# Kernel optimization log

Measured on AMD Instinct MI355X. Metric: run time of the kernel, lower is better.

## Reference

```python
import jax, jax.numpy as jnp
import numpy as np
from jax import lax


def setup_inputs() -> dict:
    key = jax.random.key(0)
    t_in = jax.random.normal(key, (16, 65536, 3), dtype=jnp.float32)
    return {"npoints": 2048, "t_in": t_in}


def reference(npoints, t_in):
    """Iterative farthest point sampling.

    t_in: (b, n, 3) float32 point coordinates.
    Returns (b, npoints) int32 indices of sampled points.
    Matches the PointNet++ CUDA kernel semantics: first sample is index 0,
    running min-distance buffer initialized to a large value, each step
    picks the argmax of the min-distance to the already-selected set.
    """
    b, n, p = t_in.shape
    assert p == 3
    BIG = jnp.float32(1e10)

    batch_ix = jnp.arange(b)

    def step(carry, _):
        dist, last_idx = carry                      # dist: (b,n), last_idx: (b,)
        last = t_in[batch_ix, last_idx]             # (b,3) last selected points
        d = jnp.sum((t_in - last[:, None, :]) ** 2, axis=-1)  # (b,n)
        dist = jnp.minimum(dist, d)
        nxt = jnp.argmax(dist, axis=-1).astype(jnp.int32)      # (b,)
        return (dist, nxt), nxt

    init_idx = jnp.zeros((b,), dtype=jnp.int32)
    dist0 = jnp.full((b, n), BIG, dtype=jnp.float32)
    (_, _), idxs = lax.scan(step, (dist0, init_idx), None, length=npoints - 1)
    # idxs: (npoints-1, b) -> (b, npoints-1)
    out = jnp.concatenate([init_idx[:, None], idxs.T], axis=1)  # (b, npoints)
    return out
```

## Files before the change

### kernel.cpp

```cpp
#include <hip/hip_runtime.h>
#include <stdint.h>


#define NBATCH   16
#define NPTS     65536
#define NPOINTS  2048
#define KBLK     16
#define THREADS  256
#define PPB      4096
#define PPT      16
#define SLOT_U64 8
#define REGION_U64 (KBLK * SLOT_U64)

#define TAGOK(w) (((unsigned)((w) >> 16) & 0xFFFFu) == tag)

typedef unsigned int uint4v __attribute__((ext_vector_type(4)));

__device__ __forceinline__ void load_slot16(const unsigned long long* p,
                                            unsigned long long& w0,
                                            unsigned long long& w1) {
    uint4v r;
    asm volatile("global_load_dwordx4 %0, %1, off sc0 sc1\n\t"
                 "s_waitcnt vmcnt(0)"
                 : "=v"(r) : "v"(p) : "memory");
    w0 = ((unsigned long long)r.y << 32) | r.x;
    w1 = ((unsigned long long)r.w << 32) | r.z;
}

__global__ __launch_bounds__(THREADS, 1)
void fps_kernel(const float* __restrict__ pts, int* __restrict__ out,
                unsigned long long* __restrict__ slots)
{
    const int bid  = blockIdx.x;
    const int g    = bid & 15;
    const int blk  = bid >> 4;
    const int tid  = threadIdx.x;
    const int lane = tid & 63;
    const int wave = tid >> 6;

    const float* __restrict__ P = pts + (size_t)g * (NPTS * 3);

    __shared__ unsigned long long s_mail[2][4];
    __shared__ unsigned long long s_cand[2][3][2];

    float  x[PPT], y[PPT], z[PPT];
    double dist[PPT];
    const int base = blk * PPB;
#pragma unroll
    for (int j = 0; j < PPT; ++j) {
        const int idx = base + j * THREADS + tid;
        x[j] = P[idx * 3 + 0];
        y[j] = P[idx * 3 + 1];
        z[j] = P[idx * 3 + 2];
        dist[j] = 1e10;
    }
    if (tid < 12) ((unsigned long long*)s_cand)[tid] = 0ull;
    if (tid < 8)  ((unsigned long long*)s_mail)[tid] = 0ull;
    __syncthreads();

    double qx = (double)P[0], qy = (double)P[1], qz = (double)P[2];
    if (blk == 0 && tid == 0) out[g * NPOINTS] = 0;

    for (int it = 0; it < NPOINTS - 1; ++it) {
        double bd = -1.0;
        int    bi = 0x7FFFFFFF;
        {
#pragma clang fp contract(off)
#pragma unroll
            for (int j = 0; j < PPT; ++j) {
                const double dx = (double)x[j] - qx;
                const double dy = (double)y[j] - qy;
                const double dz = (double)z[j] - qz;
                const double d  = (dx * dx + dy * dy) + dz * dz;
                const double nd = fmin(dist[j], d);
                dist[j] = nd;
                const bool t = nd > bd;
                bd = t ? nd : bd;
                bi = t ? (base + j * THREADS + tid) : bi;
            }
        }

#pragma unroll
        for (int m = 1; m < 64; m <<= 1) {
            const double od = __shfl_xor(bd, m, 64);
            const int    oi = __shfl_xor(bi, m, 64);
            const bool t = (od > bd) || (od == bd && oi < bi);
            bd = t ? od : bd; bi = t ? oi : bi;
        }

        const unsigned tag = (unsigned)(it + 1);
        const int par = it & 1;
        unsigned long long* rb =
            slots + (size_t)(par * NBATCH + g) * REGION_U64;

        float qxf, qyf, qzf;

        if (wave != 0) {
            if (lane == 0) {
                const unsigned long long B =
                    (unsigned long long)__double_as_longlong(bd);
                const unsigned long long TI =
                      ((unsigned long long)tag << 16)
                    | (unsigned long long)((unsigned)bi & 0xFFFFu);
                __hip_atomic_store(&s_cand[par][wave - 1][0],
                                   ((B >> 32) << 32) | TI,
                                   __ATOMIC_RELAXED,
                                   __HIP_MEMORY_SCOPE_WORKGROUP);
                __hip_atomic_store(&s_cand[par][wave - 1][1],
                                   ((B & 0xFFFFFFFFull) << 32) | TI,
                                   __ATOMIC_RELAXED,
                                   __HIP_MEMORY_SCOPE_WORKGROUP);
            }
            unsigned long long f1, f2, f3;
            int guard = 0;
            bool okm;
            do {
                f1 = __hip_atomic_load(&s_mail[par][0], __ATOMIC_RELAXED,
                                       __HIP_MEMORY_SCOPE_WORKGROUP);
                f2 = __hip_atomic_load(&s_mail[par][1], __ATOMIC_RELAXED,
                                       __HIP_MEMORY_SCOPE_WORKGROUP);
                f3 = __hip_atomic_load(&s_mail[par][2], __ATOMIC_RELAXED,
                                       __HIP_MEMORY_SCOPE_WORKGROUP);
                okm = ((unsigned)f1 == tag) & ((unsigned)f2 == tag)
                    & ((unsigned)f3 == tag);
            } while (!okm && ++guard < (1 << 20));
            qxf = __int_as_float((int)(f1 >> 32));
            qyf = __int_as_float((int)(f2 >> 32));
            qzf = __int_as_float((int)(f3 >> 32));
        } else {
            unsigned long long c[3][2];
            {
                int guard = 0;
                bool all;
                do {
                    all = true;
#pragma unroll
                    for (int w = 0; w < 3; ++w) {
                        c[w][0] = __hip_atomic_load(&s_cand[par][w][0],
                                      __ATOMIC_RELAXED,
                                      __HIP_MEMORY_SCOPE_WORKGROUP);
                        c[w][1] = __hip_atomic_load(&s_cand[par][w][1],
                                      __ATOMIC_RELAXED,
                                      __HIP_MEMORY_SCOPE_WORKGROUP);
                        all = all & TAGOK(c[w][0]) & TAGOK(c[w][1]);
                    }
                } while (!all && ++guard < (1 << 20));
            }
#pragma unroll
            for (int w = 0; w < 3; ++w) {
                const double od = __longlong_as_double((long long)(
                    ((c[w][0] >> 32) << 32) | (c[w][1] >> 32)));
                const int    oi = (int)(c[w][0] & 0xFFFFull);
                const bool t = (od > bd) || (od == bd && oi < bi);
                bd = t ? od : bd; bi = t ? oi : bi;
            }

            const unsigned long long B =
                (unsigned long long)__double_as_longlong(bd);
            const unsigned long long TI =
                  ((unsigned long long)tag << 16)
                | (unsigned long long)((unsigned)bi & 0xFFFFu);
            const unsigned long long own0 = ((B >> 32) << 32) | TI;
            const unsigned long long own1 = ((B & 0xFFFFFFFFull) << 32) | TI;

            if (lane < 2) {
                __hip_atomic_store(rb + blk * SLOT_U64 + lane,
                                   (lane == 0) ? own0 : own1,
                                   __ATOMIC_RELAXED,
                                   __HIP_MEMORY_SCOPE_AGENT);
            }

            unsigned long long* sp = rb + (lane & 15) * SLOT_U64;
            const bool own = ((lane & 15) == blk);
            unsigned long long l0 = own0, l1 = own1;
            bool ok = own;
            __builtin_amdgcn_s_sleep(12);
            int g1 = 0;
            while (!ok && g1 < 32) {
                load_slot16(sp, l0, l1);
                ok = TAGOK(l0) & TAGOK(l1);
                ++g1;
            }
            int g2 = 0;
            while (!ok) {
                l0 = __hip_atomic_load(sp + 0, __ATOMIC_RELAXED,
                                       __HIP_MEMORY_SCOPE_AGENT);
                l1 = __hip_atomic_load(sp + 1, __ATOMIC_RELAXED,
                                       __HIP_MEMORY_SCOPE_AGENT);
                ok = TAGOK(l0) & TAGOK(l1);
                if (++g2 > (1 << 20)) break;
            }

            double cd = __longlong_as_double(
                (long long)(((l0 >> 32) << 32) | (l1 >> 32)));
            int    ci = (int)(l0 & 0xFFFFull);

            const int    si = ci;
            const float* pc = P + (size_t)(unsigned)si * 3;
            const float px = pc[0];
            const float py = pc[1];
            const float pz = pc[2];

#pragma unroll
            for (int m = 1; m < 16; m <<= 1) {
                const double od = __shfl_xor(cd, m, 64);
                const int    oi = __shfl_xor(ci, m, 64);
                const bool t = (od > cd) || (od == cd && oi < ci);
                cd = t ? od : cd; ci = t ? oi : ci;
            }

            if (lane == 0 && blk == 0) out[g * NPOINTS + it + 1] = ci;

            const unsigned long long mb = __ballot(si == ci);
            const int wl = (__ffsll(mb) - 1) & 63;
            qxf = __int_as_float(
                __builtin_amdgcn_readlane(__float_as_int(px), wl));
            qyf = __int_as_float(
                __builtin_amdgcn_readlane(__float_as_int(py), wl));
            qzf = __int_as_float(
                __builtin_amdgcn_readlane(__float_as_int(pz), wl));

            if (lane < 3) {
                const unsigned coord =
                    (lane == 0) ? (unsigned)__float_as_int(qxf)
                  : (lane == 1) ? (unsigned)__float_as_int(qyf)
                                : (unsigned)__float_as_int(qzf);
                __hip_atomic_store(&s_mail[par][lane],
                                   ((unsigned long long)coord << 32)
                                 | (unsigned long long)tag,
                                   __ATOMIC_RELAXED,
                                   __HIP_MEMORY_SCOPE_WORKGROUP);
            }
        }

        qx = (double)qxf; qy = (double)qyf; qz = (double)qzf;
    }
}

extern "C" void kernel_launch(void* const* d_in, const int* in_sizes, int n_in,
                              void* d_out, int out_size, void* d_ws, size_t ws_size,
                              hipStream_t stream) {
    (void)in_sizes; (void)n_in; (void)out_size; (void)ws_size;
    const float* t_in = (const float*)d_in[1];
    int* out = (int*)d_out;
    unsigned long long* slots = (unsigned long long*)d_ws;

    dim3 grid(NBATCH * KBLK);
    dim3 block(THREADS);
    void* args[] = { (void*)&t_in, (void*)&out, (void*)&slots };
    hipLaunchCooperativeKernel((const void*)fps_kernel, grid, block, args, 0, stream);
}
```

Baseline: 4.771 ms.

## Publish per-wave candidates directly to global slots, skipping intra-block LDS merge

Each wave now writes its own argmax candidate to a global slot (16 blocks x 4 waves), and wave 0 of every block reads all 64 slots, one per lane, then reduces across the full wavefront. This drops the LDS handoff from waves 1-3 to wave 0, along with its spin wait, from the per-iteration critical path. Point coordinates are also pre-converted to double and kept in registers. The cost is four times as many global slots to poll, a full 64-lane reduction, and roughly double the register use for coordinates.

After: 4.431 ms. 1.08x faster.

```diff
diff --git a/kernel.cpp b/kernel.cpp
--- a/kernel.cpp
+++ b/kernel.cpp
@@ -9,8 +9,9 @@
 #define THREADS  256
 #define PPB      4096
 #define PPT      16
-#define SLOT_U64 8
-#define REGION_U64 (KBLK * SLOT_U64)
+#define QPB      4
+#define SLOT_U64 2
+#define REGION_U64 (KBLK * QPB * SLOT_U64)
 
 #define TAGOK(w) (((unsigned)((w) >> 16) & 0xFFFFu) == tag)
 
@@ -41,21 +42,18 @@
     const float* __restrict__ P = pts + (size_t)g * (NPTS * 3);
 
     __shared__ unsigned long long s_mail[2][4];
-    __shared__ unsigned long long s_cand[2][3][2];
-
-    float  x[PPT], y[PPT], z[PPT];
-    double dist[PPT];
+
+    double xd[PPT], yd[PPT], zd[PPT], dist[PPT];
     const int base = blk * PPB;
 #pragma unroll
     for (int j = 0; j < PPT; ++j) {
         const int idx = base + j * THREADS + tid;
-        x[j] = P[idx * 3 + 0];
-        y[j] = P[idx * 3 + 1];
-        z[j] = P[idx * 3 + 2];
+        xd[j] = (double)P[idx * 3 + 0];
+        yd[j] = (double)P[idx * 3 + 1];
+        zd[j] = (double)P[idx * 3 + 2];
         dist[j] = 1e10;
     }
-    if (tid < 12) ((unsigned long long*)s_cand)[tid] = 0ull;
-    if (tid < 8)  ((unsigned long long*)s_mail)[tid] = 0ull;
+    if (tid < 8) ((unsigned long long*)s_mail)[tid] = 0ull;
     __syncthreads();
 
     double qx = (double)P[0], qy = (double)P[1], qz = (double)P[2];
@@ -68,9 +66,9 @@
 #pragma clang fp contract(off)
 #pragma unroll
             for (int j = 0; j < PPT; ++j) {
-                const double dx = (double)x[j] - qx;
-                const double dy = (double)y[j] - qy;
-                const double dz = (double)z[j] - qz;
+                const double dx = xd[j] - qx;
+                const double dy = yd[j] - qy;
+                const double dz = zd[j] - qz;
                 const double d  = (dx * dx + dy * dy) + dz * dz;
                 const double nd = fmin(dist[j], d);
                 dist[j] = nd;
@@ -93,24 +91,24 @@
         unsigned long long* rb =
             slots + (size_t)(par * NBATCH + g) * REGION_U64;
 
+        const unsigned long long B =
+            (unsigned long long)__double_as_longlong(bd);
+        const unsigned long long TI =
+              ((unsigned long long)tag << 16)
+            | (unsigned long long)((unsigned)bi & 0xFFFFu);
+        const unsigned long long own0 = ((B >> 32) << 32) | TI;
+        const unsigned long long own1 = ((B & 0xFFFFFFFFull) << 32) | TI;
+
+        if (lane < 2) {
+            __hip_atomic_store(rb + (blk * QPB + wave) * SLOT_U64 + lane,
+                               (lane == 0) ? own0 : own1,
+                               __ATOMIC_RELAXED,
+                               __HIP_MEMORY_SCOPE_AGENT);
+        }
+
         float qxf, qyf, qzf;
 
         if (wave != 0) {
-            if (lane == 0) {
-                const unsigned long long B =
-                    (unsigned long long)__double_as_longlong(bd);
-                const unsigned long long TI =
-                      ((unsigned long long)tag << 16)
-                    | (unsigned long long)((unsigned)bi & 0xFFFFu);
-                __hip_atomic_store(&s_cand[par][wave - 1][0],
-                                   ((B >> 32) << 32) | TI,
-                                   __ATOMIC_RELAXED,
-                                   __HIP_MEMORY_SCOPE_WORKGROUP);
-                __hip_atomic_store(&s_cand[par][wave - 1][1],
-                                   ((B & 0xFFFFFFFFull) << 32) | TI,
-                                   __ATOMIC_RELAXED,
-                                   __HIP_MEMORY_SCOPE_WORKGROUP);
-            }
             unsigned long long f1, f2, f3;
             int guard = 0;
             bool okm;
@@ -128,50 +126,8 @@
             qyf = __int_as_float((int)(f2 >> 32));
             qzf = __int_as_float((int)(f3 >> 32));
         } else {
-            unsigned long long c[3][2];
-            {
-                int guard = 0;
-                bool all;
-                do {
-                    all = true;
-#pragma unroll
-                    for (int w = 0; w < 3; ++w) {
-                        c[w][0] = __hip_atomic_load(&s_cand[par][w][0],
-                                      __ATOMIC_RELAXED,
-                                      __HIP_MEMORY_SCOPE_WORKGROUP);
-                        c[w][1] = __hip_atomic_load(&s_cand[par][w][1],
-                                      __ATOMIC_RELAXED,
-                                      __HIP_MEMORY_SCOPE_WORKGROUP);
-                        all = all & TAGOK(c[w][0]) & TAGOK(c[w][1]);
-                    }
-                } while (!all && ++guard < (1 << 20));
-            }
-#pragma unroll
-            for (int w = 0; w < 3; ++w) {
-                const double od = __longlong_as_double((long long)(
-                    ((c[w][0] >> 32) << 32) | (c[w][1] >> 32)));
-                const int    oi = (int)(c[w][0] & 0xFFFFull);
-                const bool t = (od > bd) || (od == bd && oi < bi);
-                bd = t ? od : bd; bi = t ? oi : bi;
-            }
-
-            const unsigned long long B =
-                (unsigned long long)__double_as_longlong(bd);
-            const unsigned long long TI =
-                  ((unsigned long long)tag << 16)
-                | (unsigned long long)((unsigned)bi & 0xFFFFu);
-            const unsigned long long own0 = ((B >> 32) << 32) | TI;
-            const unsigned long long own1 = ((B & 0xFFFFFFFFull) << 32) | TI;
-
-            if (lane < 2) {
-                __hip_atomic_store(rb + blk * SLOT_U64 + lane,
-                                   (lane == 0) ? own0 : own1,
-                                   __ATOMIC_RELAXED,
-                                   __HIP_MEMORY_SCOPE_AGENT);
-            }
-
-            unsigned long long* sp = rb + (lane & 15) * SLOT_U64;
-            const bool own = ((lane & 15) == blk);
+            unsigned long long* sp = rb + lane * SLOT_U64;
+            const bool own = (lane == blk * QPB);
             unsigned long long l0 = own0, l1 = own1;
             bool ok = own;
             __builtin_amdgcn_s_sleep(12);
@@ -202,7 +158,7 @@
             const float pz = pc[2];
 
 #pragma unroll
-            for (int m = 1; m < 16; m <<= 1) {
+            for (int m = 1; m < 64; m <<= 1) {
                 const double od = __shfl_xor(cd, m, 64);
                 const int    oi = __shfl_xor(ci, m, 64);
                 const bool t = (od > cd) || (od == cd && oi < ci);
```
